# Performance work log

Measured on AMD Instinct MI355X. Metric: run time of the kernel, lower is better.

Reference implementation:

```python
import jax, jax.numpy as jnp
import numpy as np

N_HEADS = 16

def setup_inputs() -> dict:
    key = jax.random.key(0)
    k1, k2, k3, k4 = jax.random.split(key, 4)
    B, N, E = 4, 2048, 1024
    x = jax.random.normal(k1, (B, N, E), dtype=jnp.float32)
    s = 1.0 / np.sqrt(E)
    Wq = jax.random.normal(k2, (E, E), dtype=jnp.float32) * s
    Wk = jax.random.normal(k3, (E, E), dtype=jnp.float32) * s
    Wv = jax.random.normal(k4, (E, E), dtype=jnp.float32) * s
    return {"x": x, "Wq": Wq, "Wk": Wk, "Wv": Wv}

def reference(x, Wq, Wk, Wv):
    # first_block=False -> PositionalEncoding is identity: encoded_vectors = x
    B, N, E = x.shape
    H = N_HEADS
    D = E // H
    norm = np.sqrt(D).astype(np.float32)
    # torch nn.Linear(bias=False): y = x @ W.T
    q = (x @ Wq.T).reshape(B, N, H, D).transpose(0, 2, 1, 3)  # [B,H,N,D]
    k = (x @ Wk.T).reshape(B, N, H, D).transpose(0, 2, 1, 3)
    v = (x @ Wv.T).reshape(B, N, H, D).transpose(0, 2, 1, 3)
    scores = jnp.einsum('bhnd,bhmd->bhnm', q, k) / norm  # [B,H,N,N]
    attn = jax.nn.softmax(scores, axis=-1)
    # original einsum 'stuu, stuv -> stuv': diagonal of attn scales values
    diag = jnp.diagonal(attn, axis1=-2, axis2=-1)  # [B,H,N]
    av = diag[..., None] * v  # [B,H,N,D]
    av = av.transpose(0, 2, 1, 3).reshape(B, N, E)
    return (av, x)
```

## Files before the change

kernel.cpp:

```cpp
#include <hip/hip_runtime.h>
#include <hip/hip_bf16.h>
#include <stdint.h>

typedef __attribute__((ext_vector_type(8))) short short8;
typedef __attribute__((ext_vector_type(4))) float f32x4;

#define BATCH 4
#define SEQ   2048
#define EMB   1024
#define HEADS 16
#define DHEAD 64
#define MROWS (BATCH * SEQ)
#define NW    (EMB * EMB)

#define QSCALE 0.18033688011112042f

__device__ inline unsigned short f2bf(float f) {
    unsigned int u = __float_as_uint(f);
    unsigned int r = (u + 0x7fffu + ((u >> 16) & 1u)) >> 16;
    return (unsigned short)r;
}

__device__ __forceinline__ void gl_lds16(const short* g, short* l) {
    __builtin_amdgcn_global_load_lds(
        (const __attribute__((address_space(1))) void*)g,
        (__attribute__((address_space(3))) void*)l, 16, 0, 0);
}

template <int N>
__device__ __forceinline__ void waitvm() {
    asm volatile("s_waitcnt vmcnt(%0)" :: "n"(N) : "memory");
}

__global__ __launch_bounds__(256) void pack_all(const float* __restrict__ x,
                                                const float* __restrict__ wq,
                                                const float* __restrict__ wk,
                                                const float* __restrict__ wv,
                                                unsigned short* __restrict__ xb,
                                                unsigned short* __restrict__ wb,
                                                float* __restrict__ pass) {
    const int i = (blockIdx.x * 256 + threadIdx.x) * 8;
    const float* src;
    unsigned short* dst;
    bool isx = i < MROWS * EMB;
    if (isx) {
        src = x + i;
        dst = xb + i;
    } else {
        const int j = i - MROWS * EMB;
        src = (j < NW) ? wq + j : (j < 2 * NW) ? wk + (j - NW) : wv + (j - 2 * NW);
        dst = wb + j;
    }
    const float4* s = reinterpret_cast<const float4*>(src);
    float4 f0 = s[0];
    float4 f1 = s[1];
    union { unsigned short u[8]; short8 v; } o;
    o.u[0] = f2bf(f0.x); o.u[1] = f2bf(f0.y); o.u[2] = f2bf(f0.z); o.u[3] = f2bf(f0.w);
    o.u[4] = f2bf(f1.x); o.u[5] = f2bf(f1.y); o.u[6] = f2bf(f1.z); o.u[7] = f2bf(f1.w);
    *reinterpret_cast<short8*>(dst) = o.v;
    if (isx) {
        float4* p = reinterpret_cast<float4*>(pass + i);
        p[0] = f0;
        p[1] = f1;
    }
}

template <int MODE>
__global__ __launch_bounds__(512, 2) void gemm8(const short* __restrict__ A,
                                                const short* __restrict__ Bm,
                                                unsigned short* __restrict__ Cb,
                                                float* __restrict__ out,
                                                const float* __restrict__ dgp) {
    constexpr int K = EMB;
    constexpr int NT = K / 32;
    constexpr int BN = (MODE == 0) ? 256 : 128;
    constexpr int NF = BN / 64;
    constexpr int BUFSTRIDE = 8192 + BN * 32;
    constexpr int VW = 2 + BN / 128;

    __shared__ short Ks[3 * BUFSTRIDE];

    const int t = threadIdx.x;
    const int lane = t & 63;
    const int w = t >> 6;
    const int wr = w >> 2;
    const int wc = w & 3;
    const int rl = lane & 15;
    const int pg = (lane >> 4) ^ (lane & 3);
    const int m0 = blockIdx.x * 256;
    const int n0 = blockIdx.y * BN;

    const int sr = t >> 2;
    const int sg = (t & 3) ^ (sr & 3);
    const int soff = sr * K + sg * 8;
    const short* gA0 = A + (size_t)(m0)*K + soff;
    const short* gA1 = A + (size_t)(m0 + 128) * K + soff;
    const short* gB0 = Bm + (size_t)(n0)*K + soff;
    const short* gB1 = Bm + (size_t)(n0 + 128) * K + soff;
    short* ldsw = Ks + w * 512;

#define STAGE8(kk, bb)                                               \
    {                                                                \
        const int _k = (kk)*32;                                      \
        short* _l = ldsw + (bb)*BUFSTRIDE;                           \
        gl_lds16(gA0 + _k, _l);                                      \
        gl_lds16(gA1 + _k, _l + 4096);                               \
        gl_lds16(gB0 + _k, _l + 8192);                               \
        if (MODE == 0) gl_lds16(gB1 + _k, _l + 12288);               \
    }

    f32x4 acc[8][NF] = {};

    STAGE8(0, 0);
    STAGE8(1, 1);
    waitvm<VW>();
    __builtin_amdgcn_s_barrier();

    int cur = 0;
    for (int kt = 0; kt < NT; ++kt) {
        const int pf = kt + 2;
        if (pf < NT) {
            int nb = cur + 2; if (nb >= 3) nb -= 3;
            STAGE8(pf, nb);
        }

        const short* bufp = Ks + cur * BUFSTRIDE;
        short8 av[8], bv[NF];
#pragma unroll
        for (int i = 0; i < 8; i++)
            av[i] = *(const short8*)&bufp[wr * 4096 + i * 512 + rl * 32 + pg * 8];
#pragma unroll
        for (int j = 0; j < NF; j++) {
            const int brow = (MODE == 0) ? ((wc & 1) * 64 + j * 16 + rl)
                                         : (wc * 32 + j * 16 + rl);
            const int bh = (MODE == 0) ? (wc >> 1) : 0;
            bv[j] = *(const short8*)&bufp[8192 + bh * 4096 + brow * 32 + pg * 8];
        }

        __builtin_amdgcn_s_setprio(1);
#pragma unroll
        for (int i = 0; i < 8; i++)
#pragma unroll
            for (int j = 0; j < NF; j++)
                acc[i][j] = __builtin_amdgcn_mfma_f32_16x16x32_bf16(av[i], bv[j], acc[i][j], 0, 0, 0);
        __builtin_amdgcn_s_setprio(0);

        if (kt < NT - 2) waitvm<VW>();
        else             waitvm<0>();
        __builtin_amdgcn_s_barrier();

        cur += 1; if (cur == 3) cur = 0;
    }
#undef STAGE8

    const int gr_base = m0 + wr * 128 + (lane >> 4) * 4;
    const int gc_base = n0 + wc * (BN / 4) + rl;
#pragma unroll
    for (int i = 0; i < 8; i++) {
#pragma unroll
        for (int j = 0; j < NF; j++) {
            const int col = gc_base + j * 16;
#pragma unroll
            for (int r = 0; r < 4; r++) {
                const int grow = gr_base + i * 16 + r;
                const int bb = grow >> 11;
                const int nn = grow & 2047;
                if (MODE == 0) {
                    const int sel = col >> 10;
                    const int cc = col & 1023;
                    const int hh = cc >> 6;
                    const int dd = cc & 63;
                    const float sc = sel ? 1.0f : QSCALE;
                    Cb[(((size_t)((sel << 6) + (bb << 4) + hh) * SEQ + nn) << 6) + dd] =
                        f2bf(acc[i][j][r] * sc);
                } else {
                    const int hh = col >> 6;
                    const float d = dgp[((bb << 4) + hh) * SEQ + nn];
                    out[(size_t)grow * EMB + col] = acc[i][j][r] * d;
                }
            }
        }
    }
}

#define DNT (SEQ / 128)

__global__ __launch_bounds__(512, 4) void diag_kernel(const short* __restrict__ Qh,
                                                      const short* __restrict__ Kh,
                                                      float* __restrict__ dgp) {
    const int n = blockIdx.x;
    const int bh = (n & 7) | ((n >> 6) << 3);
    const int qt = (n >> 3) & 7;
    __shared__ short Ksd[3 * 8192];

    const int t = threadIdx.x;
    const int lane = t & 63;
    const int w = t >> 6;
    const int rl = lane & 15;
    const int g = lane >> 4;
    const int kq = g * 8;

    const short* Kbh = Kh + (size_t)bh * SEQ * DHEAD;
    const short* Qbh = Qh + (size_t)bh * SEQ * DHEAD;

    const int qbase = qt * 256 + w * 32;
    short8 a0[2], a1[2];
#pragma unroll
    for (int i = 0; i < 2; i++) {
        const int qrow = qbase + i * 16 + rl;
        a0[i] = *(const short8*)(Qbh + qrow * DHEAD + kq);
        a1[i] = *(const short8*)(Qbh + qrow * DHEAD + kq + 32);
    }

    float sdiag[2];
    const int rr = rl - g * 4;
#pragma unroll
    for (int i = 0; i < 2; i++) {
        const int krow = qbase + i * 16 + rl;
        const short8 b0d = *(const short8*)(Kbh + krow * DHEAD + kq);
        const short8 b1d = *(const short8*)(Kbh + krow * DHEAD + kq + 32);
        f32x4 cd = {};
        cd = __builtin_amdgcn_mfma_f32_16x16x32_bf16(a0[i], b0d, cd, 0, 0, 0);
        cd = __builtin_amdgcn_mfma_f32_16x16x32_bf16(a1[i], b1d, cd, 0, 0, 0);
        sdiag[i] = (rr >= 0 && rr < 4) ? cd[rr] : 0.f;
    }

    const int sr = t >> 3;
    const int sb = ((t & 7) ^ (sr & 7)) * 8;
    const short* gK0 = Kbh + sr * DHEAD + sb;
    const short* gK1 = Kbh + (sr + 64) * DHEAD + sb;
    short* ldsw = Ksd + w * 512;

#define DSTAGE(kk, bb)                                    \
    {                                                     \
        gl_lds16(gK0 + (kk)*8192, ldsw + (bb)*8192);      \
        gl_lds16(gK1 + (kk)*8192, ldsw + (bb)*8192 + 4096); \
    }

    const int blk0 = (g ^ (lane & 7)) * 8;
    const int blk1 = ((g + 4) ^ (lane & 7)) * 8;

    float ssum[2][4] = {};

    DSTAGE(0, 0);
    DSTAGE(1, 1);
    waitvm<2>();
    __builtin_amdgcn_s_barrier();

#define QKMFMA(sub, c)                                                          \
    {                                                                           \
        const short* _r = bufp + ((sub)*16 + rl) * 64;                          \
        const short8 _b0 = *(const short8*)(_r + blk0);                         \
        const short8 _b1 = *(const short8*)(_r + blk1);                         \
        c[0] = __builtin_amdgcn_mfma_f32_16x16x32_bf16(a0[0], _b0, f32x4{}, 0, 0, 0); \
        c[0] = __builtin_amdgcn_mfma_f32_16x16x32_bf16(a1[0], _b1, c[0], 0, 0, 0);    \
        c[1] = __builtin_amdgcn_mfma_f32_16x16x32_bf16(a0[1], _b0, f32x4{}, 0, 0, 0); \
        c[1] = __builtin_amdgcn_mfma_f32_16x16x32_bf16(a1[1], _b1, c[1], 0, 0, 0);    \
    }
#define EXPACC(c)                                         \
    {                                                     \
        _Pragma("unroll") for (int i = 0; i < 2; i++)     \
        _Pragma("unroll") for (int r = 0; r < 4; ++r)     \
            ssum[i][r] += __builtin_amdgcn_exp2f(c[i][r]); \
    }

    int cur = 0;
    for (int kt = 0; kt < DNT; ++kt) {
        if (kt + 2 < DNT) {
            int nb = cur + 2; if (nb >= 3) nb -= 3;
            DSTAGE(kt + 2, nb);
        }
        const short* bufp = Ksd + cur * 8192;

        f32x4 cE[2], cO[2];
        QKMFMA(0, cE);
        QKMFMA(1, cO);
        EXPACC(cE);
        QKMFMA(2, cE);
        EXPACC(cO);
        QKMFMA(3, cO);
        EXPACC(cE);
        QKMFMA(4, cE);
        EXPACC(cO);
        QKMFMA(5, cO);
        EXPACC(cE);
        QKMFMA(6, cE);
        EXPACC(cO);
        QKMFMA(7, cO);
        EXPACC(cE);
        EXPACC(cO);

        if (kt < DNT - 1) {
            if (kt < DNT - 2) waitvm<2>();
            else              waitvm<0>();
            __builtin_amdgcn_s_barrier();
        }
        cur += 1; if (cur == 3) cur = 0;
    }
#undef DSTAGE
#undef QKMFMA
#undef EXPACC

#pragma unroll
    for (int i = 0; i < 2; i++)
#pragma unroll
        for (int r = 0; r < 4; r++) {
            float v = ssum[i][r];
            v += __shfl_xor(v, 1);
            v += __shfl_xor(v, 2);
            v += __shfl_xor(v, 4);
            v += __shfl_xor(v, 8);
            ssum[i][r] = v;
        }

    if (rr >= 0 && rr < 4) {
#pragma unroll
        for (int i = 0; i < 2; i++) {
            const float dg = __builtin_amdgcn_exp2f(sdiag[i]) / ssum[i][rr];
            dgp[bh * SEQ + qbase + i * 16 + rl] = dg;
        }
    }
}

extern "C" void kernel_launch(void* const* d_in, const int* in_sizes, int n_in,
                              void* d_out, int out_size, void* d_ws, size_t ws_size,
                              hipStream_t stream) {
    const float* x  = (const float*)d_in[0];
    const float* Wq = (const float*)d_in[1];
    const float* Wk = (const float*)d_in[2];
    const float* Wv = (const float*)d_in[3];
    float* out = (float*)d_out;
    char* ws = (char*)d_ws;

    const size_t xb_off  = 0;
    const size_t wq_off  = xb_off + (size_t)MROWS * EMB * 2;
    const size_t wk_off  = wq_off + (size_t)NW * 2;
    const size_t wv_off  = wk_off + (size_t)NW * 2;
    const size_t q_off   = wv_off + (size_t)NW * 2;
    const size_t k_off   = q_off + (size_t)MROWS * EMB * 2;
    const size_t dg_off  = k_off + (size_t)MROWS * EMB * 2;

    short* xb  = (short*)(ws + xb_off);
    short* wqb = (short*)(ws + wq_off);
    short* wvb = (short*)(ws + wv_off);
    short* Qh  = (short*)(ws + q_off);
    short* Kh  = (short*)(ws + k_off);
    float* dgp = (float*)(ws + dg_off);

    const int npack = (MROWS * EMB + 3 * NW) / 2048;

    pack_all<<<npack, 256, 0, stream>>>(x, Wq, Wk, Wv,
                                        (unsigned short*)xb, (unsigned short*)wqb,
                                        out + (size_t)MROWS * EMB);

    gemm8<0><<<dim3(MROWS / 256, 2048 / 256), 512, 0, stream>>>(
        xb, wqb, (unsigned short*)Qh, nullptr, nullptr);

    diag_kernel<<<BATCH * HEADS * (SEQ / 256), 512, 0, stream>>>(Qh, Kh, dgp);

    gemm8<1><<<dim3(MROWS / 256, EMB / 128), 512, 0, stream>>>(
        xb, wvb, nullptr, out, dgp);
}
```

Before: 128.9 us.

## Split diag softmax key range across two blocks and combine partial sums in gemm

The diagonal softmax kernel now splits the key sequence in half, launching twice as many blocks (1024), each summing exponentials over 1024 keys. Partial denominators and the diagonal numerator are written to workspace, and the V-projection epilogue combines them with a division. The key staging changes from triple to double buffering with a full wait each step. The aim is to fill the GPU better with more blocks, at the cost of extra workspace traffic, less load/compute overlap, and a redundant diagonal computation per split.

```diff
diff --git a/kernel.cpp b/kernel.cpp
--- a/kernel.cpp
+++ b/kernel.cpp
@@ -70,7 +70,8 @@
                                                 const short* __restrict__ Bm,
                                                 unsigned short* __restrict__ Cb,
                                                 float* __restrict__ out,
-                                                const float* __restrict__ dgp) {
+                                                const float* __restrict__ num,
+                                                const float* __restrict__ pp) {
     constexpr int K = EMB;
     constexpr int NT = K / 32;
     constexpr int BN = (MODE == 0) ? 256 : 128;
@@ -175,7 +176,8 @@
                         f2bf(acc[i][j][r] * sc);
                 } else {
                     const int hh = col >> 6;
-                    const float d = dgp[((bb << 4) + hh) * SEQ + nn];
+                    const int idx = ((bb << 4) + hh) * SEQ + nn;
+                    const float d = num[idx] / (pp[idx] + pp[idx + 64 * SEQ]);
                     out[(size_t)grow * EMB + col] = acc[i][j][r] * d;
                 }
             }
@@ -183,15 +185,15 @@
     }
 }
 
-#define DNT (SEQ / 128)
-
 __global__ __launch_bounds__(512, 4) void diag_kernel(const short* __restrict__ Qh,
                                                       const short* __restrict__ Kh,
-                                                      float* __restrict__ dgp) {
+                                                      float* __restrict__ num,
+                                                      float* __restrict__ pp) {
     const int n = blockIdx.x;
-    const int bh = (n & 7) | ((n >> 6) << 3);
+    const int bh = (n & 7) | ((n >> 7) << 3);
     const int qt = (n >> 3) & 7;
-    __shared__ short Ksd[3 * 8192];
+    const int ks = (n >> 6) & 1;
+    __shared__ short Ksd[2 * 8192];
 
     const int t = threadIdx.x;
     const int lane = t & 63;
@@ -227,14 +229,14 @@
 
     const int sr = t >> 3;
     const int sb = ((t & 7) ^ (sr & 7)) * 8;
-    const short* gK0 = Kbh + sr * DHEAD + sb;
-    const short* gK1 = Kbh + (sr + 64) * DHEAD + sb;
+    const short* gK0 = Kbh + (size_t)ks * (SEQ / 2) * DHEAD + sr * DHEAD + sb;
+    const short* gK1 = gK0 + 64 * DHEAD;
     short* ldsw = Ksd + w * 512;
 
-#define DSTAGE(kk, bb)                                    \
-    {                                                     \
-        gl_lds16(gK0 + (kk)*8192, ldsw + (bb)*8192);      \
-        gl_lds16(gK1 + (kk)*8192, ldsw + (bb)*8192 + 4096); \
+#define DSTAGE(kk, bb)                                       \
+    {                                                        \
+        gl_lds16(gK0 + (kk)*8192, ldsw + (bb)*8192);         \
+        gl_lds16(gK1 + (kk)*8192, ldsw + (bb)*8192 + 4096);  \
     }
 
     const int blk0 = (g ^ (lane & 7)) * 8;
@@ -243,8 +245,7 @@
     float ssum[2][4] = {};
 
     DSTAGE(0, 0);
-    DSTAGE(1, 1);
-    waitvm<2>();
+    waitvm<0>();
     __builtin_amdgcn_s_barrier();
 
 #define QKMFMA(sub, c)                                                          \
@@ -264,13 +265,9 @@
             ssum[i][r] += __builtin_amdgcn_exp2f(c[i][r]); \
     }
 
-    int cur = 0;
-    for (int kt = 0; kt < DNT; ++kt) {
-        if (kt + 2 < DNT) {
-            int nb = cur + 2; if (nb >= 3) nb -= 3;
-            DSTAGE(kt + 2, nb);
-        }
-        const short* bufp = Ksd + cur * 8192;
+    for (int kt = 0; kt < 8; ++kt) {
+        if (kt < 7) DSTAGE(kt + 1, (kt + 1) & 1);
+        const short* bufp = Ksd + (kt & 1) * 8192;
 
         f32x4 cE[2], cO[2];
         QKMFMA(0, cE);
@@ -290,12 +287,10 @@
         EXPACC(cE);
         EXPACC(cO);
 
-        if (kt < DNT - 1) {
-            if (kt < DNT - 2) waitvm<2>();
-            else              waitvm<0>();
+        if (kt < 7) {
+            waitvm<0>();
             __builtin_amdgcn_s_barrier();
         }
-        cur += 1; if (cur == 3) cur = 0;
     }
 #undef DSTAGE
 #undef QKMFMA
@@ -316,8 +311,9 @@
     if (rr >= 0 && rr < 4) {
 #pragma unroll
         for (int i = 0; i < 2; i++) {
-            const float dg = __builtin_amdgcn_exp2f(sdiag[i]) / ssum[i][rr];
-            dgp[bh * SEQ + qbase + i * 16 + rl] = dg;
+            const int q = qbase + i * 16 + rl;
+            pp[(ks * 64 + bh) * SEQ + q] = ssum[i][rr];
+            if (ks == 0) num[bh * SEQ + q] = __builtin_amdgcn_exp2f(sdiag[i]);
         }
     }
 }
@@ -338,14 +334,16 @@
     const size_t wv_off  = wk_off + (size_t)NW * 2;
     const size_t q_off   = wv_off + (size_t)NW * 2;
     const size_t k_off   = q_off + (size_t)MROWS * EMB * 2;
-    const size_t dg_off  = k_off + (size_t)MROWS * EMB * 2;
+    const size_t num_off = k_off + (size_t)MROWS * EMB * 2;
+    const size_t pp_off  = num_off + (size_t)64 * SEQ * 4;
 
     short* xb  = (short*)(ws + xb_off);
     short* wqb = (short*)(ws + wq_off);
     short* wvb = (short*)(ws + wv_off);
     short* Qh  = (short*)(ws + q_off);
     short* Kh  = (short*)(ws + k_off);
-    float* dgp = (float*)(ws + dg_off);
+    float* num = (float*)(ws + num_off);
+    float* pp  = (float*)(ws + pp_off);
 
     const int npack = (MROWS * EMB + 3 * NW) / 2048;
 
@@ -354,10 +352,10 @@
                                         out + (size_t)MROWS * EMB);
 
     gemm8<0><<<dim3(MROWS / 256, 2048 / 256), 512, 0, stream>>>(
-        xb, wqb, (unsigned short*)Qh, nullptr, nullptr);
-
-    diag_kernel<<<BATCH * HEADS * (SEQ / 256), 512, 0, stream>>>(Qh, Kh, dgp);
+        xb, wqb, (unsigned short*)Qh, nullptr, nullptr, nullptr);
+
+    diag_kernel<<<1024, 512, 0, stream>>>(Qh, Kh, num, pp);
 
     gemm8<1><<<dim3(MROWS / 256, EMB / 128), 512, 0, stream>>>(
-        xb, wvb, nullptr, out, dgp);
-}
+        xb, wvb, nullptr, out, num, pp);
+}
```

Measured after the change: 131.1 us. Within noise of the previous version (+1.7%).

## Drop LDS staging in diag kernel; load K directly into registers

Applied to the files above, without the earlier changes.

The diag softmax-denominator kernel no longer stages K tiles through a triple-buffered LDS ring with barriers. Each wave now loads K fragments straight from global memory into registers, software-pipelined two steps ahead. Blocks shrink to 256 threads, and each wave handles 64 query rows instead of 32, so every K fragment feeds four Q fragments. This removes LDS traffic and barrier syncs, but every wave re-reads K from global or L2 without sharing, and register pressure rises.

```diff
diff --git a/kernel.cpp b/kernel.cpp
--- a/kernel.cpp
+++ b/kernel.cpp
@@ -183,16 +183,12 @@
     }
 }
 
-#define DNT (SEQ / 128)
-
-__global__ __launch_bounds__(512, 4) void diag_kernel(const short* __restrict__ Qh,
+__global__ __launch_bounds__(256, 2) void diag_kernel(const short* __restrict__ Qh,
                                                       const short* __restrict__ Kh,
                                                       float* __restrict__ dgp) {
     const int n = blockIdx.x;
     const int bh = (n & 7) | ((n >> 6) << 3);
     const int qt = (n >> 3) & 7;
-    __shared__ short Ksd[3 * 8192];
-
     const int t = threadIdx.x;
     const int lane = t & 63;
     const int w = t >> 6;
@@ -203,19 +199,19 @@
     const short* Kbh = Kh + (size_t)bh * SEQ * DHEAD;
     const short* Qbh = Qh + (size_t)bh * SEQ * DHEAD;
 
-    const int qbase = qt * 256 + w * 32;
-    short8 a0[2], a1[2];
-#pragma unroll
-    for (int i = 0; i < 2; i++) {
+    const int qbase = qt * 256 + w * 64;
+    short8 a0[4], a1[4];
+#pragma unroll
+    for (int i = 0; i < 4; i++) {
         const int qrow = qbase + i * 16 + rl;
         a0[i] = *(const short8*)(Qbh + qrow * DHEAD + kq);
         a1[i] = *(const short8*)(Qbh + qrow * DHEAD + kq + 32);
     }
 
-    float sdiag[2];
+    float sdiag[4];
     const int rr = rl - g * 4;
 #pragma unroll
-    for (int i = 0; i < 2; i++) {
+    for (int i = 0; i < 4; i++) {
         const int krow = qbase + i * 16 + rl;
         const short8 b0d = *(const short8*)(Kbh + krow * DHEAD + kq);
         const short8 b1d = *(const short8*)(Kbh + krow * DHEAD + kq + 32);
@@ -225,84 +221,46 @@
         sdiag[i] = (rr >= 0 && rr < 4) ? cd[rr] : 0.f;
     }
 
-    const int sr = t >> 3;
-    const int sb = ((t & 7) ^ (sr & 7)) * 8;
-    const short* gK0 = Kbh + sr * DHEAD + sb;
-    const short* gK1 = Kbh + (sr + 64) * DHEAD + sb;
-    short* ldsw = Ksd + w * 512;
-
-#define DSTAGE(kk, bb)                                    \
-    {                                                     \
-        gl_lds16(gK0 + (kk)*8192, ldsw + (bb)*8192);      \
-        gl_lds16(gK1 + (kk)*8192, ldsw + (bb)*8192 + 4096); \
-    }
-
-    const int blk0 = (g ^ (lane & 7)) * 8;
-    const int blk1 = ((g + 4) ^ (lane & 7)) * 8;
-
-    float ssum[2][4] = {};
-
-    DSTAGE(0, 0);
-    DSTAGE(1, 1);
-    waitvm<2>();
-    __builtin_amdgcn_s_barrier();
-
-#define QKMFMA(sub, c)                                                          \
-    {                                                                           \
-        const short* _r = bufp + ((sub)*16 + rl) * 64;                          \
-        const short8 _b0 = *(const short8*)(_r + blk0);                         \
-        const short8 _b1 = *(const short8*)(_r + blk1);                         \
-        c[0] = __builtin_amdgcn_mfma_f32_16x16x32_bf16(a0[0], _b0, f32x4{}, 0, 0, 0); \
-        c[0] = __builtin_amdgcn_mfma_f32_16x16x32_bf16(a1[0], _b1, c[0], 0, 0, 0);    \
-        c[1] = __builtin_amdgcn_mfma_f32_16x16x32_bf16(a0[1], _b0, f32x4{}, 0, 0, 0); \
-        c[1] = __builtin_amdgcn_mfma_f32_16x16x32_bf16(a1[1], _b1, c[1], 0, 0, 0);    \
-    }
-#define EXPACC(c)                                         \
-    {                                                     \
-        _Pragma("unroll") for (int i = 0; i < 2; i++)     \
-        _Pragma("unroll") for (int r = 0; r < 4; ++r)     \
-            ssum[i][r] += __builtin_amdgcn_exp2f(c[i][r]); \
-    }
-
-    int cur = 0;
-    for (int kt = 0; kt < DNT; ++kt) {
-        if (kt + 2 < DNT) {
-            int nb = cur + 2; if (nb >= 3) nb -= 3;
-            DSTAGE(kt + 2, nb);
-        }
-        const short* bufp = Ksd + cur * 8192;
-
-        f32x4 cE[2], cO[2];
-        QKMFMA(0, cE);
-        QKMFMA(1, cO);
-        EXPACC(cE);
-        QKMFMA(2, cE);
-        EXPACC(cO);
-        QKMFMA(3, cO);
-        EXPACC(cE);
-        QKMFMA(4, cE);
-        EXPACC(cO);
-        QKMFMA(5, cO);
-        EXPACC(cE);
-        QKMFMA(6, cE);
-        EXPACC(cO);
-        QKMFMA(7, cO);
-        EXPACC(cE);
-        EXPACC(cO);
-
-        if (kt < DNT - 1) {
-            if (kt < DNT - 2) waitvm<2>();
-            else              waitvm<0>();
-            __builtin_amdgcn_s_barrier();
-        }
-        cur += 1; if (cur == 3) cur = 0;
-    }
-#undef DSTAGE
-#undef QKMFMA
-#undef EXPACC
-
-#pragma unroll
-    for (int i = 0; i < 2; i++)
+    const short* kp = Kbh + rl * DHEAD + kq;
+
+#define LOADS(s, b0v, b1v)                                      \
+    {                                                           \
+        const short* _p = kp + (s) * (16 * DHEAD);              \
+        b0v = *(const short8*)_p;                               \
+        b1v = *(const short8*)(_p + 32);                        \
+    }
+#define COMP(b0v, b1v)                                                              \
+    {                                                                               \
+        _Pragma("unroll") for (int i = 0; i < 4; i++) {                             \
+            f32x4 c;                                                               \
+            c = __builtin_amdgcn_mfma_f32_16x16x32_bf16(a0[i], b0v, f32x4{}, 0, 0, 0); \
+            c = __builtin_amdgcn_mfma_f32_16x16x32_bf16(a1[i], b1v, c, 0, 0, 0);    \
+            _Pragma("unroll") for (int r = 0; r < 4; ++r)                           \
+                ssum[i][r] += __builtin_amdgcn_exp2f(c[r]);                         \
+        }                                                                           \
+    }
+
+    float ssum[4][4] = {};
+
+    short8 eb0, eb1, ob0, ob1;
+    LOADS(0, eb0, eb1);
+    LOADS(1, ob0, ob1);
+    for (int s = 0; s < 126; s += 2) {
+        short8 n0, n1, m0, m1;
+        LOADS(s + 2, n0, n1);
+        LOADS(s + 3, m0, m1);
+        COMP(eb0, eb1);
+        COMP(ob0, ob1);
+        eb0 = n0; eb1 = n1;
+        ob0 = m0; ob1 = m1;
+    }
+    COMP(eb0, eb1);
+    COMP(ob0, ob1);
+#undef LOADS
+#undef COMP
+
+#pragma unroll
+    for (int i = 0; i < 4; i++)
 #pragma unroll
         for (int r = 0; r < 4; r++) {
             float v = ssum[i][r];
@@ -315,7 +273,7 @@
 
     if (rr >= 0 && rr < 4) {
 #pragma unroll
-        for (int i = 0; i < 2; i++) {
+        for (int i = 0; i < 4; i++) {
             const float dg = __builtin_amdgcn_exp2f(sdiag[i]) / ssum[i][rr];
             dgp[bh * SEQ + qbase + i * 16 + rl] = dg;
         }
@@ -356,7 +314,7 @@
     gemm8<0><<<dim3(MROWS / 256, 2048 / 256), 512, 0, stream>>>(
         xb, wqb, (unsigned short*)Qh, nullptr, nullptr);
 
-    diag_kernel<<<BATCH * HEADS * (SEQ / 256), 512, 0, stream>>>(Qh, Kh, dgp);
+    diag_kernel<<<512, 256, 0, stream>>>(Qh, Kh, dgp);
 
     gemm8<1><<<dim3(MROWS / 256, EMB / 128), 512, 0, stream>>>(
         xb, wvb, nullptr, out, dgp);
```

Result: slower. 150.4 us (+16.7%).
